# Kernel optimization log

Hardware: AMD Instinct MI355X
Metric: run time of the kernel (lower is better)

The kernel has to match this reference:

```python
import jax, jax.numpy as jnp
import numpy as np

N = 50000      # nodes
E = 800000     # directed edges
GNN_DIM = 128  # node feature dim
HID = 64       # per-head hidden dim of conv1
HEADS = 2
OUT = 16       # output_dim (classes)
TEXT = 500     # tf-idf text dim
M = 10000      # masked / labeled nodes


def setup_inputs() -> dict:
    key = jax.random.key(0)
    ks = jax.random.split(key, 32)
    w = lambda k, s: jax.random.normal(k, s, jnp.float32) * 0.05
    inp = {
        'text_features': jax.random.normal(ks[0], (M, TEXT), jnp.float32),
        'x': jax.random.normal(ks[1], (N, GNN_DIM), jnp.float32),
        'edge_index': jax.random.randint(ks[2], (2, E), 0, N),
        'mask': jax.random.randint(ks[3], (M,), 0, N),
        # text MLP (Linear stored as [in, out])
        'fc1_w': w(ks[4], (TEXT, 128)), 'fc1_b': w(ks[5], (128,)),
        'fc2_w': w(ks[6], (128, 64)),  'fc2_b': w(ks[7], (64,)),
        'fc3_w': w(ks[8], (64, 16)),   'fc3_b': w(ks[9], (16,)),
        'fc4_w': w(ks[10], (16, OUT)), 'fc4_b': w(ks[11], (OUT,)),
        'sc_w': w(ks[12], (TEXT, OUT)), 'sc_b': w(ks[13], (OUT,)),
        # GATConv1: in=GNN_DIM, heads=2, out=HID, concat=True
        'W1': w(ks[14], (GNN_DIM, HEADS * HID)),
        'att_src1': w(ks[15], (HEADS, HID)), 'att_dst1': w(ks[16], (HEADS, HID)),
        'b1': w(ks[17], (HEADS * HID,)),
        # GATConv2: in=2*HID, heads=1, out=OUT, concat=False
        'W2': w(ks[18], (HEADS * HID, OUT)),
        'att_src2': w(ks[19], (1, OUT)), 'att_dst2': w(ks[20], (1, OUT)),
        'b2': w(ks[21], (OUT,)),
        # fc_final: [2*OUT, OUT]
        'fcf_w': w(ks[22], (2 * OUT, OUT)), 'fcf_b': w(ks[23], (OUT,)),
    }
    return inp


def _gat_layer(h_in, src, dst, W, a_src, a_dst, b, heads, dim, concat):
    # PyG GATConv (default negative_slope=0.2, self-loops already appended)
    n = h_in.shape[0]
    h = (h_in @ W).reshape(n, heads, dim)                      # [N,H,D]
    a_s = jnp.einsum('nhd,hd->nh', h, a_src)                   # [N,H]
    a_d = jnp.einsum('nhd,hd->nh', h, a_dst)
    e = jax.nn.leaky_relu(a_s[src] + a_d[dst], 0.2)            # [E,H]
    emax = jax.ops.segment_max(e, dst, num_segments=n)
    ex = jnp.exp(e - emax[dst])
    den = jax.ops.segment_sum(ex, dst, num_segments=n)
    alpha = ex / (den[dst] + 1e-16)                            # [E,H]
    msg = h[src] * alpha[:, :, None]                           # [E,H,D]
    out = jax.ops.segment_sum(msg, dst, num_segments=n)        # [N,H,D]
    out = out.reshape(n, heads * dim) if concat else out.mean(axis=1)
    return out + b


def reference(text_features, x, edge_index, mask,
              fc1_w, fc1_b, fc2_w, fc2_b, fc3_w, fc3_b, fc4_w, fc4_b,
              sc_w, sc_b, W1, att_src1, att_dst1, b1,
              W2, att_src2, att_dst2, b2, fcf_w, fcf_b):
    n = x.shape[0]
    loop = jnp.arange(n, dtype=edge_index.dtype)
    src = jnp.concatenate([edge_index[0], loop])
    dst = jnp.concatenate([edge_index[1], loop])

    # GNN branch
    g = jax.nn.relu(_gat_layer(x, src, dst, W1, att_src1, att_dst1, b1,
                               HEADS, HID, True))
    g = _gat_layer(g, src, dst, W2, att_src2, att_dst2, b2, 1, OUT, False)
    gnn_out = g[mask]                                          # [M,OUT]

    # text MLP branch with shortcut
    t = jax.nn.relu(text_features @ fc1_w + fc1_b)
    t = jax.nn.relu(t @ fc2_w + fc2_b)
    t = jax.nn.relu(t @ fc3_w + fc3_b)
    text_out = (t @ fc4_w + fc4_b) + (text_features @ sc_w + sc_b)  # [M,OUT]

    combined = jnp.concatenate([text_out, gnn_out], axis=1)    # [M,2*OUT]
    return jax.nn.log_softmax(combined @ fcf_w + fcf_b, axis=1)
```

## Files before the change

kernel.cpp:

```cpp
#include <hip/hip_runtime.h>
#include <hip/hip_bf16.h>
#include <cmath>

#define TEXTD 500
#define GNN_DIM 128
#define DEGP(v) ((v) << 5)

typedef __attribute__((ext_vector_type(8))) short bf16x8;
typedef __attribute__((ext_vector_type(4))) float f32x4;

__device__ __forceinline__ float bf2f(unsigned short u) {
    union { unsigned int i; float f; } cv;
    cv.i = ((unsigned int)u) << 16;
    return cv.f;
}
__device__ __forceinline__ unsigned short f2b(float x) {
    __hip_bfloat16 b = __float2bfloat16(x);
    return *reinterpret_cast<unsigned short*>(&b);
}
__device__ __forceinline__ float u2f(unsigned int u) {
    union { unsigned int i; float f; } cv; cv.i = u; return cv.f;
}
__device__ __forceinline__ bf16x8 cvt8(const float* p) {
    float4 u = *(const float4*)p;
    float4 v = *(const float4*)(p + 4);
    bf16x8 f;
    f[0] = (short)f2b(u.x); f[1] = (short)f2b(u.y);
    f[2] = (short)f2b(u.z); f[3] = (short)f2b(u.w);
    f[4] = (short)f2b(v.x); f[5] = (short)f2b(v.y);
    f[6] = (short)f2b(v.z); f[7] = (short)f2b(v.w);
    return f;
}

__global__ __launch_bounds__(256) void conv_w_kernel(
    const float* __restrict__ fc1_w, const float* __restrict__ sc_w,
    const float* __restrict__ W1, const float* __restrict__ W2,
    unsigned short* __restrict__ w1cat, unsigned short* __restrict__ w1g,
    unsigned short* __restrict__ w2t)
{
    int idx = blockIdx.x * 256 + threadIdx.x;
    if (idx < 144 * 512) {
        int n = idx >> 9, k = idx & 511;
        float v = 0.f;
        if (k < TEXTD) v = (n < 128) ? fc1_w[k * 128 + n] : sc_w[k * 16 + (n - 128)];
        w1cat[idx] = f2b(v);
    } else if (idx < 144 * 512 + 128 * 128) {
        int j = idx - 144 * 512;
        int n = j >> 7, k = j & 127;
        w1g[j] = f2b(W1[k * 128 + n]);
    } else if (idx < 144 * 512 + 128 * 128 + 16 * 128) {
        int j = idx - (144 * 512 + 128 * 128);
        int n = j >> 7, k = j & 127;
        w2t[j] = f2b(W2[k * 16 + n]);
    }
}

__global__ __launch_bounds__(256) void gemm_text_kernel(
    const float* __restrict__ text, const short* __restrict__ B,
    const float* __restrict__ fc1_b, const float* __restrict__ sc_b,
    float* __restrict__ t1, float* __restrict__ tsc, int M)
{
    const int tid = threadIdx.x;
    const int wave = tid >> 6, lane = tid & 63;
    const int q = lane >> 4, col = lane & 15;
    const int mb = blockIdx.x * 64 + wave * 16;
    const int arow = min(mb + col, M - 1);
    const float* ap = text + (size_t)arow * TEXTD + q * 8;

    bf16x8 afrag[16];
    #pragma unroll
    for (int ks = 0; ks < 15; ks++) afrag[ks] = cvt8(ap + ks * 32);
    {
        bf16x8 f;
        int k0 = 480 + q * 8;
        #pragma unroll
        for (int e = 0; e < 8; e++) {
            int k = k0 + e;
            f[e] = (short)((k < TEXTD) ? f2b(text[(size_t)arow * TEXTD + k]) : 0);
        }
        afrag[15] = f;
    }

    for (int nb = 0; nb < 9; nb++) {
        const short* bp = B + (size_t)(nb * 16 + col) * 512 + q * 8;
        f32x4 acc = {0.f, 0.f, 0.f, 0.f};
        #pragma unroll
        for (int ks = 0; ks < 16; ks++)
            acc = __builtin_amdgcn_mfma_f32_16x16x32_bf16(afrag[ks], *(const bf16x8*)(bp + ks * 32), acc, 0, 0, 0);
        #pragma unroll
        for (int i = 0; i < 4; i++) {
            int row = mb + q * 4 + i;
            if (row < M) {
                if (nb < 8) t1[(size_t)row * 128 + nb * 16 + col] = fmaxf(acc[i] + fc1_b[nb * 16 + col], 0.f);
                else        tsc[(size_t)row * 16 + col] = acc[i] + sc_b[col];
            }
        }
    }
}

__global__ __launch_bounds__(256) void gemm_h1_kernel(
    const float* __restrict__ x, const short* __restrict__ B,
    const float* __restrict__ as1w, const float* __restrict__ ad1w,
    unsigned short* __restrict__ h1, float* __restrict__ a_s, float* __restrict__ a_d, int N)
{
    const int tid = threadIdx.x;
    const int wave = tid >> 6, lane = tid & 63;
    const int q = lane >> 4, col = lane & 15;
    const int mb = blockIdx.x * 64 + wave * 16;
    const int arow = min(mb + col, N - 1);
    const float* ap = x + (size_t)arow * 128 + q * 8;

    bf16x8 afrag[4];
    #pragma unroll
    for (int ks = 0; ks < 4; ks++) afrag[ks] = cvt8(ap + ks * 32);

    float ps0[4] = {0,0,0,0}, ps1[4] = {0,0,0,0};
    float pd0[4] = {0,0,0,0}, pd1[4] = {0,0,0,0};

    #pragma unroll
    for (int nb = 0; nb < 8; nb++) {
        const short* bp = B + (size_t)(nb * 16 + col) * 128 + q * 8;
        f32x4 acc = {0.f, 0.f, 0.f, 0.f};
        #pragma unroll
        for (int ks = 0; ks < 4; ks++)
            acc = __builtin_amdgcn_mfma_f32_16x16x32_bf16(afrag[ks], *(const bf16x8*)(bp + ks * 32), acc, 0, 0, 0);
        const int j = nb * 16 + col;
        const float asj = as1w[j], adj = ad1w[j];
        #pragma unroll
        for (int i = 0; i < 4; i++) {
            int row = mb + q * 4 + i;
            if (row < N) h1[(size_t)row * 128 + j] = f2b(acc[i]);
            if (nb < 4) { ps0[i] = fmaf(acc[i], asj, ps0[i]); pd0[i] = fmaf(acc[i], adj, pd0[i]); }
            else        { ps1[i] = fmaf(acc[i], asj, ps1[i]); pd1[i] = fmaf(acc[i], adj, pd1[i]); }
        }
    }
    #pragma unroll
    for (int i = 0; i < 4; i++) {
        float v0 = ps0[i], v1 = ps1[i], w0 = pd0[i], w1 = pd1[i];
        #pragma unroll
        for (int off = 1; off < 16; off <<= 1) {
            v0 += __shfl_xor(v0, off, 16);
            v1 += __shfl_xor(v1, off, 16);
            w0 += __shfl_xor(w0, off, 16);
            w1 += __shfl_xor(w1, off, 16);
        }
        int row = mb + q * 4 + i;
        if (col == 0 && row < N) {
            a_s[2 * row] = v0; a_s[2 * row + 1] = v1;
            a_d[2 * row] = w0; a_d[2 * row + 1] = w1;
        }
    }
}

__global__ __launch_bounds__(128) void text_tail_kernel(
    const float* __restrict__ t1g, const float* __restrict__ tsc,
    const float* __restrict__ fc2_w, const float* __restrict__ fc2_b,
    const float* __restrict__ fc3_w, const float* __restrict__ fc3_b,
    const float* __restrict__ fc4_w, const float* __restrict__ fc4_b,
    float* __restrict__ text_out, int M)
{
    __shared__ float t1[8][128];
    __shared__ float t2[8][64];
    __shared__ float t3[8][16];
    const int tid = threadIdx.x;
    const int m0 = blockIdx.x * 8;

    for (int r = 0; r < 8; r++) {
        int row = m0 + r;
        t1[r][tid] = (row < M) ? t1g[(size_t)row * 128 + tid] : 0.f;
    }
    __syncthreads();

    const int r2 = tid >> 6, c2 = tid & 63;
    for (int rb = 0; rb < 4; rb++) {
        int row = rb * 2 + r2;
        float a2 = fc2_b[c2];
        for (int k = 0; k < 128; k++) a2 = fmaf(t1[row][k], fc2_w[k * 64 + c2], a2);
        t2[row][c2] = fmaxf(a2, 0.f);
    }
    __syncthreads();

    const int rs = tid >> 4, cs = tid & 15;
    float a3 = fc3_b[cs];
    for (int k = 0; k < 64; k++) a3 = fmaf(t2[rs][k], fc3_w[k * 16 + cs], a3);
    t3[rs][cs] = fmaxf(a3, 0.f);
    __syncthreads();

    float a4 = fc4_b[cs];
    #pragma unroll
    for (int k = 0; k < 16; k++) a4 = fmaf(t3[rs][k], fc4_w[k * 16 + cs], a4);
    int row = m0 + rs;
    if (row < M) text_out[(size_t)row * 16 + cs] = a4 + tsc[(size_t)row * 16 + cs];
}

__global__ __launch_bounds__(256) void deg_hist_kernel(
    const int* __restrict__ edst, int* __restrict__ deg, int* __restrict__ rank, int E)
{
    const int base = blockIdx.x * 1024 + threadIdx.x;
    int e0 = base;
    int e1 = base + 256;
    int e2 = base + 512;
    int e3 = base + 768;
    int d0 = (e0 < E) ? edst[e0] : -1;
    int d1 = (e1 < E) ? edst[e1] : -1;
    int d2 = (e2 < E) ? edst[e2] : -1;
    int d3 = (e3 < E) ? edst[e3] : -1;
    int r0 = (d0 >= 0) ? atomicAdd(&deg[DEGP(d0)], 1) : 0;
    int r1 = (d1 >= 0) ? atomicAdd(&deg[DEGP(d1)], 1) : 0;
    int r2 = (d2 >= 0) ? atomicAdd(&deg[DEGP(d2)], 1) : 0;
    int r3 = (d3 >= 0) ? atomicAdd(&deg[DEGP(d3)], 1) : 0;
    if (d0 >= 0) rank[e0] = r0;
    if (d1 >= 0) rank[e1] = r1;
    if (d2 >= 0) rank[e2] = r2;
    if (d3 >= 0) rank[e3] = r3;
}

__global__ __launch_bounds__(256) void part_kernel(
    const int* __restrict__ deg, int* __restrict__ bsum, int N)
{
    const int tid = threadIdx.x;
    int i = blockIdx.x * 256 + tid;
    int d = (i < N) ? deg[DEGP(i)] + 1 : 0;
    #pragma unroll
    for (int off = 32; off > 0; off >>= 1) d += __shfl_down(d, off, 64);
    __shared__ int wsum[4];
    if ((tid & 63) == 0) wsum[tid >> 6] = d;
    __syncthreads();
    if (tid == 0) bsum[blockIdx.x] = wsum[0] + wsum[1] + wsum[2] + wsum[3];
}

__global__ __launch_bounds__(256) void scan_bsums_kernel(
    int* __restrict__ bsum, int NB)
{
    __shared__ int sc[256];
    const int tid = threadIdx.x;
    int v = (tid < NB) ? bsum[tid] : 0;
    sc[tid] = v;
    for (int off = 1; off < 256; off <<= 1) {
        __syncthreads();
        int t = (tid >= off) ? sc[tid - off] : 0;
        __syncthreads();
        sc[tid] += t;
    }
    __syncthreads();
    if (tid < NB) bsum[tid] = sc[tid] - v;
}

__global__ __launch_bounds__(256) void rowptr_kernel(
    const int* __restrict__ deg, const int* __restrict__ bsum,
    int* __restrict__ rowptr, int N)
{
    __shared__ int sc[256];
    const int tid = threadIdx.x;
    const int i = blockIdx.x * 256 + tid;
    int d = (i < N) ? deg[DEGP(i)] + 1 : 0;
    sc[tid] = d;
    for (int off = 1; off < 256; off <<= 1) {
        __syncthreads();
        int t = (tid >= off) ? sc[tid - off] : 0;
        __syncthreads();
        sc[tid] += t;
    }
    __syncthreads();
    int incl = sc[tid];
    int base = bsum[blockIdx.x];
    if (i < N) rowptr[i] = base + incl - d;
    if (i == N - 1) rowptr[N] = base + incl;
}

__device__ __forceinline__ float edge_w(float e) {
    return __expf(e > 0.f ? e : 0.2f * e);
}

__global__ __launch_bounds__(256) void fillw_kernel(
    const int* __restrict__ esrc, const int* __restrict__ edst,
    const int* __restrict__ rank, const int* __restrict__ rowptr,
    uint2* __restrict__ eslot,
    const float* __restrict__ a_s, const float* __restrict__ a_d, int E, int N)
{
    int e = blockIdx.x * 256 + threadIdx.x;
    if (e < E) {
        int src = esrc[e], dst = edst[e];
        int pos = rowptr[dst] + 1 + rank[e];
        float2 as = *(const float2*)(a_s + 2 * src);
        float2 ad = *(const float2*)(a_d + 2 * dst);
        unsigned int w0 = f2b(edge_w(as.x + ad.x));
        unsigned int w1 = f2b(edge_w(as.y + ad.y));
        uint2 o; o.x = (unsigned int)src; o.y = (w1 << 16) | w0;
        eslot[pos] = o;
    } else if (e < E + N) {
        int v = e - E;
        float2 as = *(const float2*)(a_s + 2 * v);
        float2 ad = *(const float2*)(a_d + 2 * v);
        unsigned int w0 = f2b(edge_w(as.x + ad.x));
        unsigned int w1 = f2b(edge_w(as.y + ad.y));
        uint2 o; o.x = (unsigned int)v; o.y = (w1 << 16) | w0;
        eslot[rowptr[v]] = o;
    }
}

template<int B>
__device__ __forceinline__ void gat1_batch(
    int i0, int end, int endm1, int wsh,
    const uint2* __restrict__ eslot, const uint2* __restrict__ h1u, unsigned int dp,
    float& a0, float& a1, float& a2, float& a3, float& den)
{
    int ics[B];
    uint2 sl[B];
    float wv[B];
    uint2 hv[B];
    #pragma unroll
    for (int k = 0; k < B; k++) ics[k] = min(i0 + 2 * k, endm1);
    #pragma unroll
    for (int k = 0; k < B; k++) sl[k] = eslot[ics[k]];
    #pragma unroll
    for (int k = 0; k < B; k++) {
        float w = u2f((sl[k].y << wsh) & 0xffff0000u);
        wv[k] = (i0 + 2 * k < end) ? w : 0.f;
    }
    #pragma unroll
    for (int k = 0; k < B; k++) hv[k] = h1u[(sl[k].x << 5) | dp];
    #pragma unroll
    for (int k = 0; k < B; k++) {
        float w = wv[k];
        den += w;
        a0 = fmaf(w, u2f(hv[k].x << 16),          a0);
        a1 = fmaf(w, u2f(hv[k].x & 0xffff0000u),  a1);
        a2 = fmaf(w, u2f(hv[k].y << 16),          a2);
        a3 = fmaf(w, u2f(hv[k].y & 0xffff0000u),  a3);
    }
}

__global__ __launch_bounds__(256) void gat1_gather_kernel(
    const int* __restrict__ rowptr, const uint2* __restrict__ eslot,
    const uint2* __restrict__ h1u,
    const float* __restrict__ b1, uint2* __restrict__ g1b, int N)
{
    const int v = blockIdx.x * 4 + (threadIdx.x >> 6);
    if (v >= N) return;
    const int lane = threadIdx.x & 63;
    const int slot = lane >> 5;
    const unsigned int dp = lane & 31;
    const int head = dp >> 4;
    const int wsh = head ? 0 : 16;
    const int beg = rowptr[v], end = rowptr[v + 1];
    const int deg = end - beg;
    const int endm1 = end - 1;
    const int i0 = beg + slot;

    float a0 = 0.f, a1 = 0.f, a2 = 0.f, a3 = 0.f, den = 0.f;

    if (deg <= 8) {
        gat1_batch<4>(i0, end, endm1, wsh, eslot, h1u, dp, a0, a1, a2, a3, den);
    } else {
        gat1_batch<8>(i0, end, endm1, wsh, eslot, h1u, dp, a0, a1, a2, a3, den);
        for (int base = i0 + 16; base < end; base += 8)
            gat1_batch<4>(base, end, endm1, wsh, eslot, h1u, dp, a0, a1, a2, a3, den);
    }

    a0 += __shfl_xor(a0, 32, 64);
    a1 += __shfl_xor(a1, 32, 64);
    a2 += __shfl_xor(a2, 32, 64);
    a3 += __shfl_xor(a3, 32, 64);
    den += __shfl_xor(den, 32, 64);

    if (lane < 32) {
        float inv = 1.f / (den + 1e-16f);
        float4 bv = *(const float4*)(b1 + 4 * dp);
        float o0 = fmaxf(fmaf(a0, inv, bv.x), 0.f);
        float o1 = fmaxf(fmaf(a1, inv, bv.y), 0.f);
        float o2 = fmaxf(fmaf(a2, inv, bv.z), 0.f);
        float o3 = fmaxf(fmaf(a3, inv, bv.w), 0.f);
        uint2 o;
        o.x = ((unsigned int)f2b(o1) << 16) | f2b(o0);
        o.y = ((unsigned int)f2b(o3) << 16) | f2b(o2);
        g1b[((unsigned int)v << 5) | dp] = o;
    }
}

__global__ __launch_bounds__(256) void gat2_proj_kernel(
    const unsigned short* __restrict__ g1b, const short* __restrict__ w2t,
    const float* __restrict__ as2w, const float* __restrict__ ad2w,
    float* __restrict__ h2, float* __restrict__ a_s2, float* __restrict__ a_d2, int N)
{
    const int tid = threadIdx.x;
    const int wave = tid >> 6, lane = tid & 63;
    const int q = lane >> 4, col = lane & 15;
    const int mb = blockIdx.x * 64 + wave * 16;
    const int arow = min(mb + col, N - 1);
    const short* ap = (const short*)g1b + (size_t)arow * 128 + q * 8;
    const short* bp = w2t + (size_t)col * 128 + q * 8;

    f32x4 acc = {0.f, 0.f, 0.f, 0.f};
    #pragma unroll
    for (int ks = 0; ks < 4; ks++)
        acc = __builtin_amdgcn_mfma_f32_16x16x32_bf16(
            *(const bf16x8*)(ap + ks * 32), *(const bf16x8*)(bp + ks * 32), acc, 0, 0, 0);

    const float asj = as2w[col], adj = ad2w[col];
    #pragma unroll
    for (int i = 0; i < 4; i++) {
        int row = mb + q * 4 + i;
        float ps = acc[i] * asj, pd = acc[i] * adj;
        #pragma unroll
        for (int off = 1; off < 16; off <<= 1) {
            ps += __shfl_xor(ps, off, 16);
            pd += __shfl_xor(pd, off, 16);
        }
        if (row < N) {
            h2[(size_t)row * 16 + col] = acc[i];
            if (col == 0) { a_s2[row] = ps; a_d2[row] = pd; }
        }
    }
}

__global__ __launch_bounds__(256) void gat2_gather_kernel(
    const int* __restrict__ rowptr, const uint2* __restrict__ eslot,
    const float* __restrict__ h2,
    const float* __restrict__ a_s2, const float* __restrict__ a_d2,
    const float* __restrict__ b2, const int* __restrict__ mask,
    float* __restrict__ g2m, int M)
{
    const int tid = threadIdx.x;
    const int m = blockIdx.x * 4 + (tid >> 6);
    if (m >= M) return;
    const int lane = tid & 63, slot = lane >> 4, c = lane & 15;
    const int v = mask[m];
    const float adv = a_d2[v];
    const int beg = rowptr[v], end = rowptr[v + 1];
    const int i0 = beg + slot;

    float acc = 0.f, den = 0.f;
    unsigned int idxs[8];
    float msk[8], as_[8], hval[8];
    #pragma unroll
    for (int k = 0; k < 8; k++) {
        int i = i0 + 4 * k;
        int ic = min(i, end - 1);
        idxs[k] = eslot[ic].x;
        msk[k] = (i < end) ? 1.f : 0.f;
    }
    #pragma unroll
    for (int k = 0; k < 8; k++) as_[k] = a_s2[idxs[k]];
    #pragma unroll
    for (int k = 0; k < 8; k++) hval[k] = h2[(idxs[k] << 4) | (unsigned)c];
    #pragma unroll
    for (int k = 0; k < 8; k++) {
        float e = as_[k] + adv;
        float w = msk[k] * __expf(e > 0.f ? e : 0.2f * e);
        den += w;
        acc = fmaf(w, hval[k], acc);
    }
    for (int i = i0 + 32; i < end; i += 4) {
        unsigned int src = eslot[i].x;
        float e = a_s2[src] + adv;
        float w = __expf(e > 0.f ? e : 0.2f * e);
        den += w;
        acc = fmaf(w, h2[(src << 4) | (unsigned)c], acc);
    }

    acc += __shfl_xor(acc, 16, 64);
    acc += __shfl_xor(acc, 32, 64);
    den += __shfl_xor(den, 16, 64);
    den += __shfl_xor(den, 32, 64);
    if (slot == 0) g2m[(size_t)m * 16 + c] = acc / (den + 1e-16f) + b2[c];
}

__global__ __launch_bounds__(64) void final_kernel(
    const float* __restrict__ text_out, const float* __restrict__ g2m,
    const float* __restrict__ fcf_w, const float* __restrict__ fcf_b,
    float* __restrict__ out, int M)
{
    const int lane = threadIdx.x;
    const int g = lane >> 4, j = lane & 15;
    const int m = blockIdx.x * 4 + g;
    if (m >= M) return;

    float tval = text_out[(size_t)m * 16 + j];
    float gval = g2m[(size_t)m * 16 + j];

    float logit = fcf_b[j];
    #pragma unroll
    for (int k = 0; k < 16; k++) {
        logit = fmaf(__shfl(tval, k, 16), fcf_w[k * 16 + j], logit);
        logit = fmaf(__shfl(gval, k, 16), fcf_w[(16 + k) * 16 + j], logit);
    }
    float mx = logit;
    #pragma unroll
    for (int off = 8; off > 0; off >>= 1) mx = fmaxf(mx, __shfl_xor(mx, off, 16));
    float se = expf(logit - mx);
    #pragma unroll
    for (int off = 8; off > 0; off >>= 1) se += __shfl_xor(se, off, 16);
    out[(size_t)m * 16 + j] = logit - mx - logf(se);
}

extern "C" void kernel_launch(void* const* d_in, const int* in_sizes, int n_in,
                              void* d_out, int out_size, void* d_ws, size_t ws_size,
                              hipStream_t stream)
{
    const float* text  = (const float*)d_in[0];
    const float* x     = (const float*)d_in[1];
    const int*   ei    = (const int*)  d_in[2];
    const int*   mask  = (const int*)  d_in[3];
    const float* fc1_w = (const float*)d_in[4];  const float* fc1_b = (const float*)d_in[5];
    const float* fc2_w = (const float*)d_in[6];  const float* fc2_b = (const float*)d_in[7];
    const float* fc3_w = (const float*)d_in[8];  const float* fc3_b = (const float*)d_in[9];
    const float* fc4_w = (const float*)d_in[10]; const float* fc4_b = (const float*)d_in[11];
    const float* sc_w  = (const float*)d_in[12]; const float* sc_b  = (const float*)d_in[13];
    const float* W1    = (const float*)d_in[14];
    const float* as1w  = (const float*)d_in[15]; const float* ad1w  = (const float*)d_in[16];
    const float* b1    = (const float*)d_in[17];
    const float* W2    = (const float*)d_in[18];
    const float* as2w  = (const float*)d_in[19]; const float* ad2w  = (const float*)d_in[20];
    const float* b2    = (const float*)d_in[21];
    const float* fcf_w = (const float*)d_in[22]; const float* fcf_b = (const float*)d_in[23];

    const int M  = in_sizes[3];
    const int N  = in_sizes[1] / GNN_DIM;
    const int E  = in_sizes[2] / 2;
    const int EP = E + N;
    const int* esrc = ei;
    const int* edst = ei + E;

    const int Mp = ((M + 63) / 64) * 64;
    const int Np = ((N + 63) / 64) * 64;
    const int NB = (N + 255) / 256;

    float* ws = (float*)d_ws;
    size_t off = 0;
    auto alloc = [&](size_t n) { float* p = ws + off; off += (n + 63) & ~size_t(63); return p; };

    unsigned short* h1    = (unsigned short*)alloc((size_t)Np * 64);
    unsigned int*   g1b   = (unsigned int*)  alloc((size_t)N * 64);
    unsigned short* w1cat = (unsigned short*)alloc(144 * 256);
    unsigned short* w1g   = (unsigned short*)alloc(128 * 64);
    unsigned short* w2t   = (unsigned short*)alloc(16 * 64);
    float* t1       = alloc((size_t)M * 128);
    float* tsc      = alloc((size_t)M * 16);
    float* a_s1     = alloc((size_t)2 * N);
    float* a_d1     = alloc((size_t)2 * N);
    float* h2       = alloc((size_t)N * 16);
    float* a_s2     = alloc(N);
    float* a_d2     = alloc(N);
    float* text_out = alloc((size_t)M * 16);
    float* g2m      = alloc((size_t)M * 16);
    uint2* eslot    = (uint2*)alloc((size_t)2 * EP);
    int* deg        = (int*)alloc((size_t)N * 32);
    int* rank       = (int*)alloc(E);
    int* rowptr     = (int*)alloc(N + 1);
    int* bsum       = (int*)alloc(256);

    hipMemsetAsync(deg, 0, (size_t)N * 32 * sizeof(int), stream);
    deg_hist_kernel<<<(E + 1023) / 1024, 256, 0, stream>>>(edst, deg, rank, E);
    part_kernel<<<NB, 256, 0, stream>>>(deg, bsum, N);
    scan_bsums_kernel<<<1, 256, 0, stream>>>(bsum, NB);
    rowptr_kernel<<<NB, 256, 0, stream>>>(deg, bsum, rowptr, N);

    conv_w_kernel<<<(144 * 512 + 128 * 128 + 16 * 128 + 255) / 256, 256, 0, stream>>>(
        fc1_w, sc_w, W1, W2, w1cat, w1g, w2t);

    gemm_h1_kernel<<<Np / 64, 256, 0, stream>>>(
        x, (const short*)w1g, as1w, ad1w, h1, a_s1, a_d1, N);

    fillw_kernel<<<(E + N + 255) / 256, 256, 0, stream>>>(
        esrc, edst, rank, rowptr, eslot, a_s1, a_d1, E, N);

    gemm_text_kernel<<<Mp / 64, 256, 0, stream>>>(
        text, (const short*)w1cat, fc1_b, sc_b, t1, tsc, M);
    text_tail_kernel<<<(M + 7) / 8, 128, 0, stream>>>(
        t1, tsc, fc2_w, fc2_b, fc3_w, fc3_b, fc4_w, fc4_b, text_out, M);

    gat1_gather_kernel<<<(N + 3) / 4, 256, 0, stream>>>(
        rowptr, eslot, (const uint2*)h1, b1, (uint2*)g1b, N);

    gat2_proj_kernel<<<Np / 64, 256, 0, stream>>>(
        (const unsigned short*)g1b, (const short*)w2t, as2w, ad2w, h2, a_s2, a_d2, N);

    gat2_gather_kernel<<<(M + 3) / 4, 256, 0, stream>>>(
        rowptr, eslot, h2, a_s2, a_d2, b2, mask, g2m, M);

    final_kernel<<<(M + 3) / 4, 64, 0, stream>>>(
        text_out, g2m, fcf_w, fcf_b, (float*)d_out, M);
}
```

Baseline: 200.5 us.

## Fuse kernels to cut launches: setup+memset, text MLP, scan, gat2+final

Folds the degree memset into the weight-conversion kernel, merges the block-sum scan into rowptr_kernel (each block rescans the sums redundantly), fuses the text GEMM with the MLP tail through shared memory, and fuses the GAT2 gather with the final linear+log_softmax. This removes four launches and the global round trips for t1, tsc and g2m. The fused text kernel uses about 57KB of shared memory per block, which may lower occupancy, and its tail matmuls run over 64 rows per block.

```diff
diff --git a/kernel.cpp b/kernel.cpp
--- a/kernel.cpp
+++ b/kernel.cpp
@@ -32,13 +32,19 @@
     return f;
 }
 
-__global__ __launch_bounds__(256) void conv_w_kernel(
+__global__ __launch_bounds__(256) void setup_kernel(
+    int* __restrict__ deg, int N, int NB,
     const float* __restrict__ fc1_w, const float* __restrict__ sc_w,
     const float* __restrict__ W1, const float* __restrict__ W2,
     unsigned short* __restrict__ w1cat, unsigned short* __restrict__ w1g,
     unsigned short* __restrict__ w2t)
 {
-    int idx = blockIdx.x * 256 + threadIdx.x;
+    if ((int)blockIdx.x < NB) {
+        int v = blockIdx.x * 256 + threadIdx.x;
+        if (v < N) deg[DEGP(v)] = 0;
+        return;
+    }
+    int idx = (blockIdx.x - NB) * 256 + threadIdx.x;
     if (idx < 144 * 512) {
         int n = idx >> 9, k = idx & 511;
         float v = 0.f;
@@ -55,16 +61,25 @@
     }
 }
 
-__global__ __launch_bounds__(256) void gemm_text_kernel(
+__global__ __launch_bounds__(256) void text_fused_kernel(
     const float* __restrict__ text, const short* __restrict__ B,
     const float* __restrict__ fc1_b, const float* __restrict__ sc_b,
-    float* __restrict__ t1, float* __restrict__ tsc, int M)
-{
+    const float* __restrict__ fc2_w, const float* __restrict__ fc2_b,
+    const float* __restrict__ fc3_w, const float* __restrict__ fc3_b,
+    const float* __restrict__ fc4_w, const float* __restrict__ fc4_b,
+    float* __restrict__ text_out, int M)
+{
+    __shared__ float t1s[64][128];
+    __shared__ float tscs[64][16];
+    __shared__ float t2s[64][64];
+    __shared__ float t3s[64][16];
+
     const int tid = threadIdx.x;
     const int wave = tid >> 6, lane = tid & 63;
     const int q = lane >> 4, col = lane & 15;
-    const int mb = blockIdx.x * 64 + wave * 16;
-    const int arow = min(mb + col, M - 1);
+    const int mb = blockIdx.x * 64;
+    const int rbase = wave * 16;
+    const int arow = min(mb + rbase + col, M - 1);
     const float* ap = text + (size_t)arow * TEXTD + q * 8;
 
     bf16x8 afrag[16];
@@ -89,12 +104,38 @@
             acc = __builtin_amdgcn_mfma_f32_16x16x32_bf16(afrag[ks], *(const bf16x8*)(bp + ks * 32), acc, 0, 0, 0);
         #pragma unroll
         for (int i = 0; i < 4; i++) {
-            int row = mb + q * 4 + i;
-            if (row < M) {
-                if (nb < 8) t1[(size_t)row * 128 + nb * 16 + col] = fmaxf(acc[i] + fc1_b[nb * 16 + col], 0.f);
-                else        tsc[(size_t)row * 16 + col] = acc[i] + sc_b[col];
-            }
-        }
+            int rl = rbase + q * 4 + i;
+            if (nb < 8) t1s[rl][nb * 16 + col] = fmaxf(acc[i] + fc1_b[nb * 16 + col], 0.f);
+            else        tscs[rl][col] = acc[i] + sc_b[col];
+        }
+    }
+    __syncthreads();
+
+    const int c2 = tid & 63, rg2 = tid >> 6;
+    for (int rb = 0; rb < 16; rb++) {
+        int row = rb * 4 + rg2;
+        float a2 = fc2_b[c2];
+        for (int k = 0; k < 128; k++) a2 = fmaf(t1s[row][k], fc2_w[k * 64 + c2], a2);
+        t2s[row][c2] = fmaxf(a2, 0.f);
+    }
+    __syncthreads();
+
+    const int cs = tid & 15, rg3 = tid >> 4;
+    for (int rb = 0; rb < 4; rb++) {
+        int row = rb * 16 + rg3;
+        float a3 = fc3_b[cs];
+        for (int k = 0; k < 64; k++) a3 = fmaf(t2s[row][k], fc3_w[k * 16 + cs], a3);
+        t3s[row][cs] = fmaxf(a3, 0.f);
+    }
+    __syncthreads();
+
+    for (int rb = 0; rb < 4; rb++) {
+        int row = rb * 16 + rg3;
+        float a4 = fc4_b[cs];
+        #pragma unroll
+        for (int k = 0; k < 16; k++) a4 = fmaf(t3s[row][k], fc4_w[k * 16 + cs], a4);
+        int rg = mb + row;
+        if (rg < M) text_out[(size_t)rg * 16 + cs] = a4 + tscs[row][cs];
     }
 }
 
@@ -150,47 +191,6 @@
             a_d[2 * row] = w0; a_d[2 * row + 1] = w1;
         }
     }
-}
-
-__global__ __launch_bounds__(128) void text_tail_kernel(
-    const float* __restrict__ t1g, const float* __restrict__ tsc,
-    const float* __restrict__ fc2_w, const float* __restrict__ fc2_b,
-    const float* __restrict__ fc3_w, const float* __restrict__ fc3_b,
-    const float* __restrict__ fc4_w, const float* __restrict__ fc4_b,
-    float* __restrict__ text_out, int M)
-{
-    __shared__ float t1[8][128];
-    __shared__ float t2[8][64];
-    __shared__ float t3[8][16];
-    const int tid = threadIdx.x;
-    const int m0 = blockIdx.x * 8;
-
-    for (int r = 0; r < 8; r++) {
-        int row = m0 + r;
-        t1[r][tid] = (row < M) ? t1g[(size_t)row * 128 + tid] : 0.f;
-    }
-    __syncthreads();
-
-    const int r2 = tid >> 6, c2 = tid & 63;
-    for (int rb = 0; rb < 4; rb++) {
-        int row = rb * 2 + r2;
-        float a2 = fc2_b[c2];
-        for (int k = 0; k < 128; k++) a2 = fmaf(t1[row][k], fc2_w[k * 64 + c2], a2);
-        t2[row][c2] = fmaxf(a2, 0.f);
-    }
-    __syncthreads();
-
-    const int rs = tid >> 4, cs = tid & 15;
-    float a3 = fc3_b[cs];
-    for (int k = 0; k < 64; k++) a3 = fmaf(t2[rs][k], fc3_w[k * 16 + cs], a3);
-    t3[rs][cs] = fmaxf(a3, 0.f);
-    __syncthreads();
-
-    float a4 = fc4_b[cs];
-    #pragma unroll
-    for (int k = 0; k < 16; k++) a4 = fmaf(t3[rs][k], fc4_w[k * 16 + cs], a4);
-    int row = m0 + rs;
-    if (row < M) text_out[(size_t)row * 16 + cs] = a4 + tsc[(size_t)row * 16 + cs];
 }
 
 __global__ __launch_bounds__(256) void deg_hist_kernel(
@@ -229,29 +229,25 @@
     if (tid == 0) bsum[blockIdx.x] = wsum[0] + wsum[1] + wsum[2] + wsum[3];
 }
 
-__global__ __launch_bounds__(256) void scan_bsums_kernel(
-    int* __restrict__ bsum, int NB)
-{
+__global__ __launch_bounds__(256) void rowptr_kernel(
+    const int* __restrict__ deg, const int* __restrict__ bsum,
+    int* __restrict__ rowptr, int N, int NB)
+{
+    __shared__ int bsc[256];
     __shared__ int sc[256];
     const int tid = threadIdx.x;
-    int v = (tid < NB) ? bsum[tid] : 0;
-    sc[tid] = v;
+
+    int bv = (tid < NB) ? bsum[tid] : 0;
+    bsc[tid] = bv;
     for (int off = 1; off < 256; off <<= 1) {
         __syncthreads();
-        int t = (tid >= off) ? sc[tid - off] : 0;
+        int t = (tid >= off) ? bsc[tid - off] : 0;
         __syncthreads();
-        sc[tid] += t;
+        bsc[tid] += t;
     }
     __syncthreads();
-    if (tid < NB) bsum[tid] = sc[tid] - v;
-}
-
-__global__ __launch_bounds__(256) void rowptr_kernel(
-    const int* __restrict__ deg, const int* __restrict__ bsum,
-    int* __restrict__ rowptr, int N)
-{
-    __shared__ int sc[256];
-    const int tid = threadIdx.x;
+    const int base = (blockIdx.x == 0) ? 0 : bsc[blockIdx.x - 1];
+
     const int i = blockIdx.x * 256 + tid;
     int d = (i < N) ? deg[DEGP(i)] + 1 : 0;
     sc[tid] = d;
@@ -263,7 +259,6 @@
     }
     __syncthreads();
     int incl = sc[tid];
-    int base = bsum[blockIdx.x];
     if (i < N) rowptr[i] = base + incl - d;
     if (i == N - 1) rowptr[N] = base + incl;
 }
@@ -414,12 +409,14 @@
     }
 }
 
-__global__ __launch_bounds__(256) void gat2_gather_kernel(
+__global__ __launch_bounds__(256) void gat2_final_kernel(
     const int* __restrict__ rowptr, const uint2* __restrict__ eslot,
     const float* __restrict__ h2,
     const float* __restrict__ a_s2, const float* __restrict__ a_d2,
     const float* __restrict__ b2, const int* __restrict__ mask,
-    float* __restrict__ g2m, int M)
+    const float* __restrict__ text_out,
+    const float* __restrict__ fcf_w, const float* __restrict__ fcf_b,
+    float* __restrict__ out, int M)
 {
     const int tid = threadIdx.x;
     const int m = blockIdx.x * 4 + (tid >> 6);
@@ -463,35 +460,25 @@
     acc += __shfl_xor(acc, 32, 64);
     den += __shfl_xor(den, 16, 64);
     den += __shfl_xor(den, 32, 64);
-    if (slot == 0) g2m[(size_t)m * 16 + c] = acc / (den + 1e-16f) + b2[c];
-}
-
-__global__ __launch_bounds__(64) void final_kernel(
-    const float* __restrict__ text_out, const float* __restrict__ g2m,
-    const float* __restrict__ fcf_w, const float* __restrict__ fcf_b,
-    float* __restrict__ out, int M)
-{
-    const int lane = threadIdx.x;
-    const int g = lane >> 4, j = lane & 15;
-    const int m = blockIdx.x * 4 + g;
-    if (m >= M) return;
-
-    float tval = text_out[(size_t)m * 16 + j];
-    float gval = g2m[(size_t)m * 16 + j];
-
-    float logit = fcf_b[j];
-    #pragma unroll
-    for (int k = 0; k < 16; k++) {
-        logit = fmaf(__shfl(tval, k, 16), fcf_w[k * 16 + j], logit);
-        logit = fmaf(__shfl(gval, k, 16), fcf_w[(16 + k) * 16 + j], logit);
-    }
-    float mx = logit;
-    #pragma unroll
-    for (int off = 8; off > 0; off >>= 1) mx = fmaxf(mx, __shfl_xor(mx, off, 16));
-    float se = expf(logit - mx);
-    #pragma unroll
-    for (int off = 8; off > 0; off >>= 1) se += __shfl_xor(se, off, 16);
-    out[(size_t)m * 16 + j] = logit - mx - logf(se);
+
+    if (slot == 0) {
+        float gval = acc / (den + 1e-16f) + b2[c];
+        float tval = text_out[(size_t)m * 16 + c];
+
+        float logit = fcf_b[c];
+        #pragma unroll
+        for (int k = 0; k < 16; k++) {
+            logit = fmaf(__shfl(tval, k, 16), fcf_w[k * 16 + c], logit);
+            logit = fmaf(__shfl(gval, k, 16), fcf_w[(16 + k) * 16 + c], logit);
+        }
+        float mx = logit;
+        #pragma unroll
+        for (int off = 8; off > 0; off >>= 1) mx = fmaxf(mx, __shfl_xor(mx, off, 16));
+        float se = expf(logit - mx);
+        #pragma unroll
+        for (int off = 8; off > 0; off >>= 1) se += __shfl_xor(se, off, 16);
+        out[(size_t)m * 16 + c] = logit - mx - logf(se);
+    }
 }
 
 extern "C" void kernel_launch(void* const* d_in, const int* in_sizes, int n_in,
@@ -535,29 +522,26 @@
     unsigned short* w1cat = (unsigned short*)alloc(144 * 256);
     unsigned short* w1g   = (unsigned short*)alloc(128 * 64);
     unsigned short* w2t   = (unsigned short*)alloc(16 * 64);
-    float* t1       = alloc((size_t)M * 128);
-    float* tsc      = alloc((size_t)M * 16);
     float* a_s1     = alloc((size_t)2 * N);
     float* a_d1     = alloc((size_t)2 * N);
     float* h2       = alloc((size_t)N * 16);
     float* a_s2     = alloc(N);
     float* a_d2     = alloc(N);
     float* text_out = alloc((size_t)M * 16);
-    float* g2m      = alloc((size_t)M * 16);
     uint2* eslot    = (uint2*)alloc((size_t)2 * EP);
     int* deg        = (int*)alloc((size_t)N * 32);
     int* rank       = (int*)alloc(E);
     int* rowptr     = (int*)alloc(N + 1);
     int* bsum       = (int*)alloc(256);
 
-    hipMemsetAsync(deg, 0, (size_t)N * 32 * sizeof(int), stream);
+    const int convBlocks = (144 * 512 + 128 * 128 + 16 * 128 + 255) / 256;
+
+    setup_kernel<<<NB + convBlocks, 256, 0, stream>>>(
+        deg, N, NB, fc1_w, sc_w, W1, W2, w1cat, w1g, w2t);
+
     deg_hist_kernel<<<(E + 1023) / 1024, 256, 0, stream>>>(edst, deg, rank, E);
     part_kernel<<<NB, 256, 0, stream>>>(deg, bsum, N);
-    scan_bsums_kernel<<<1, 256, 0, stream>>>(bsum, NB);
-    rowptr_kernel<<<NB, 256, 0, stream>>>(deg, bsum, rowptr, N);
-
-    conv_w_kernel<<<(144 * 512 + 128 * 128 + 16 * 128 + 255) / 256, 256, 0, stream>>>(
-        fc1_w, sc_w, W1, W2, w1cat, w1g, w2t);
+    rowptr_kernel<<<NB, 256, 0, stream>>>(deg, bsum, rowptr, N, NB);
 
     gemm_h1_kernel<<<Np / 64, 256, 0, stream>>>(
         x, (const short*)w1g, as1w, ad1w, h1, a_s1, a_d1, N);
@@ -565,10 +549,9 @@
     fillw_kernel<<<(E + N + 255) / 256, 256, 0, stream>>>(
         esrc, edst, rank, rowptr, eslot, a_s1, a_d1, E, N);
 
-    gemm_text_kernel<<<Mp / 64, 256, 0, stream>>>(
-        text, (const short*)w1cat, fc1_b, sc_b, t1, tsc, M);
-    text_tail_kernel<<<(M + 7) / 8, 128, 0, stream>>>(
-        t1, tsc, fc2_w, fc2_b, fc3_w, fc3_b, fc4_w, fc4_b, text_out, M);
+    text_fused_kernel<<<Mp / 64, 256, 0, stream>>>(
+        text, (const short*)w1cat, fc1_b, sc_b,
+        fc2_w, fc2_b, fc3_w, fc3_b, fc4_w, fc4_b, text_out, M);
 
     gat1_gather_kernel<<<(N + 3) / 4, 256, 0, stream>>>(
         rowptr, eslot, (const uint2*)h1, b1, (uint2*)g1b, N);
@@ -576,9 +559,7 @@
     gat2_proj_kernel<<<Np / 64, 256, 0, stream>>>(
         (const unsigned short*)g1b, (const short*)w2t, as2w, ad2w, h2, a_s2, a_d2, N);
 
-    gat2_gather_kernel<<<(M + 3) / 4, 256, 0, stream>>>(
-        rowptr, eslot, h2, a_s2, a_d2, b2, mask, g2m, M);
-
-    final_kernel<<<(M + 3) / 4, 64, 0, stream>>>(
-        text_out, g2m, fcf_w, fcf_b, (float*)d_out, M);
-}
+    gat2_final_kernel<<<(M + 3) / 4, 256, 0, stream>>>(
+        rowptr, eslot, h2, a_s2, a_d2, b2, mask, text_out, fcf_w, fcf_b,
+        (float*)d_out, M);
+}
```

New measurement: 189.3 us. -5.6%, faster.
